# Performance work log

Measured on AMD Instinct MI355X. Metric: run time of the kernel, lower is better.

## Reference

```python
import jax, jax.numpy as jnp
import numpy as np

B, N, C, L = 32, 1024, 1024, 16  # batch, pixels (HW), channels, visual tokens


def setup_inputs() -> dict:
    key = jax.random.key(0)
    ks = jax.random.split(key, 18)
    s = lambda fan_in: 1.0 / np.sqrt(fan_in)
    def lin(kw, kb, fin, fout):
        W = jax.random.uniform(kw, (fin, fout), jnp.float32, -s(fin), s(fin))
        b = jax.random.uniform(kb, (fout,), jnp.float32, -s(fin), s(fin))
        return W, b
    tok_W, tok_b = lin(ks[0], ks[1], C, L)          # tokenizer pointwise conv
    key_W, key_b = lin(ks[2], ks[3], C, C // 2)     # transformer key proj
    query_W, query_b = lin(ks[4], ks[5], C, C // 2) # transformer query proj
    f1_W, f1_b = lin(ks[6], ks[7], C, C)            # FFN 1
    f2_W, f2_b = lin(ks[8], ks[9], C, C)            # FFN 2
    q_W, q_b = lin(ks[10], ks[11], C, C)            # projector W_q
    k_W, k_b = lin(ks[12], ks[13], C, C)            # projector W_k
    feature_map = jax.random.normal(ks[14], (B, N, C), jnp.float32)
    T_in = jnp.zeros((B, L, C), jnp.float32)  # unused by FilterBasedTokenizer
    return dict(feature_map=feature_map, T_in=T_in,
                tok_W=tok_W, tok_b=tok_b, key_W=key_W, key_b=key_b,
                query_W=query_W, query_b=query_b, f1_W=f1_W, f1_b=f1_b,
                f2_W=f2_W, f2_b=f2_b, q_W=q_W, q_b=q_b, k_W=k_W, k_b=k_b)


def reference(feature_map, T_in, tok_W, tok_b, key_W, key_b, query_W, query_b,
              f1_W, f1_b, f2_W, f2_b, q_W, q_b, k_W, k_b):
    X = feature_map  # [B, N, C]
    # --- FilterBasedTokenizer: softmax over pixel dim, aggregate pixels -> tokens
    proj = X @ tok_W + tok_b                         # [B, N, L]
    attn = jax.nn.softmax(proj, axis=1)              # softmax over N (dim=1)
    T = jnp.einsum('bnl,bnc->blc', attn, X)          # [B, L, C]
    # --- Transformer block on visual tokens
    k = T @ key_W + key_b                            # [B, L, C/2]
    q = T @ query_W + query_b                        # [B, L, C/2]
    scores = jnp.einsum('bld,bmd->blm', k, q)        # [B, L, L]
    T_dash = T + jax.nn.softmax(scores, axis=2) @ T  # self-attn residual
    T_out = T_dash + (jax.nn.relu(T_dash @ f1_W + f1_b) @ f2_W + f2_b)
    # --- Projector: pixels attend to tokens
    sim = jnp.einsum('bnc,blc->bnl', X @ q_W + q_b, T_out @ k_W + k_b)  # [B, N, L]
    X_out = X + jax.nn.softmax(sim, axis=2) @ T_out  # [B, N, C]
    return (X_out, T_out)
```

## Files before the change

### kernel.cpp

```cpp
#include <hip/hip_runtime.h>
#include <hip/hip_bf16.h>
#include <stdint.h>

#define BB 32
#define NN 1024
#define CC 1024
#define LL 16

typedef __attribute__((ext_vector_type(4))) float f32x4;
typedef __attribute__((ext_vector_type(8))) short short8;
typedef __attribute__((ext_vector_type(4))) unsigned short ushort4v;

__device__ __forceinline__ unsigned short f2bf(float f) {
  union { float f; unsigned u; } v; v.f = f;
  unsigned r = v.u + 0x7FFF + ((v.u >> 16) & 1);
  return (unsigned short)(r >> 16);
}
__device__ __forceinline__ float bf2f(unsigned short h) {
  union { unsigned u; float f; } v; v.u = ((unsigned)h) << 16; return v.f;
}

__global__ __launch_bounds__(256) void wprep(
    const float* __restrict__ keyW, const float* __restrict__ queryW,
    const float* __restrict__ f1W, const float* __restrict__ f2W,
    const float* __restrict__ kW, const float* __restrict__ qW,
    const float* __restrict__ tokW, const float* __restrict__ keyb,
    const float* __restrict__ queryb,
    unsigned short* __restrict__ WkqT, unsigned short* __restrict__ f1WT,
    unsigned short* __restrict__ f2WT, unsigned short* __restrict__ kWT,
    unsigned short* __restrict__ qWbf, unsigned short* __restrict__ tokWT,
    float* __restrict__ biaskq)
{
  int z = blockIdx.z;
  int tx = threadIdx.x, ty = threadIdx.y;
  if (z == 5) {
    int gid = (blockIdx.y * 32 + blockIdx.x) * 256 + ty * 32 + tx;
    if (gid < 16384) {
      int l = gid >> 10, c = gid & 1023;
      tokWT[gid] = f2bf(tokW[c * 16 + l]);
    } else if (gid < 17408) {
      int i = gid - 16384;
      biaskq[i] = (i < 512) ? keyb[i] : queryb[i - 512];
    }
    return;
  }
  if (z == 4) {
#pragma unroll
    for (int i = 0; i < 4; ++i) {
      int row = blockIdx.y * 32 + ty + 8 * i;
      int col = blockIdx.x * 32 + tx;
      qWbf[row * 1024 + col] = f2bf(qW[row * 1024 + col]);
    }
    return;
  }
  __shared__ float tile[32][33];
  int j0 = blockIdx.x * 32, k0 = blockIdx.y * 32;
  const float* src = (z == 1) ? f1W : (z == 2) ? f2W : kW;
#pragma unroll
  for (int i = 0; i < 4; ++i) {
    int k = k0 + ty + 8 * i;
    int j = j0 + tx;
    float v;
    if (z == 0) v = (j < 512) ? keyW[k * 512 + j] : queryW[k * 512 + (j - 512)];
    else        v = src[k * 1024 + j];
    tile[ty + 8 * i][tx] = v;
  }
  __syncthreads();
  unsigned short* dst = (z == 0) ? WkqT : (z == 1) ? f1WT : (z == 2) ? f2WT : kWT;
#pragma unroll
  for (int i = 0; i < 4; ++i) {
    int j = j0 + ty + 8 * i;
    dst[j * 1024 + k0 + tx] = f2bf(tile[tx][ty + 8 * i]);
  }
}

__global__ __launch_bounds__(256) void proj_mfma(
    const float* __restrict__ X, const unsigned short* __restrict__ Wt,
    const float* __restrict__ bias, float* __restrict__ out)
{
  __shared__ __align__(16) char sp[16384];
  int tid = threadIdx.x, wid = tid >> 6, lane = tid & 63;
  int lr = lane & 15, hi = lane >> 4;
  int pix0 = blockIdx.x * 64;
  int b = pix0 >> 10;
  int row = tid >> 2, seg = tid & 3;
  const float* xr = X + (size_t)(pix0 + row) * 1024 + seg * 32;
  const unsigned short* Wb = Wt + (size_t)lr * 1024 + hi * 8;
  int wbyte[4];
#pragma unroll
  for (int u = 0; u < 4; ++u)
    wbyte[u] = row * 256 + (((seg * 64 + u * 16) ^ ((row & 7) << 4)));
  int arow = wid * 16 + lr;
  int rbyte = arow * 256;
  int rx = (arow & 7) << 4;
  f32x4 acc = (f32x4)0.f;
  for (int k0 = 0; k0 < 1024; k0 += 128) {
    f32x4 v[8];
#pragma unroll
    for (int i = 0; i < 8; ++i) v[i] = *(const f32x4*)(xr + k0 + i * 4);
    __syncthreads();
#pragma unroll
    for (int u = 0; u < 4; ++u) {
      short8 pk;
      pk[0] = (short)f2bf(v[2*u][0]);   pk[1] = (short)f2bf(v[2*u][1]);
      pk[2] = (short)f2bf(v[2*u][2]);   pk[3] = (short)f2bf(v[2*u][3]);
      pk[4] = (short)f2bf(v[2*u+1][0]); pk[5] = (short)f2bf(v[2*u+1][1]);
      pk[6] = (short)f2bf(v[2*u+1][2]); pk[7] = (short)f2bf(v[2*u+1][3]);
      *(short8*)(sp + wbyte[u]) = pk;
    }
    __syncthreads();
#pragma unroll
    for (int kk = 0; kk < 4; ++kk) {
      short8 af = *(const short8*)(sp + rbyte + (((kk * 64 + hi * 16) ^ rx)));
      short8 bf = *(const short8*)(Wb + k0 + kk * 32);
      acc = __builtin_amdgcn_mfma_f32_16x16x32_bf16(af, bf, acc, 0, 0, 0);
    }
  }
  int pixb = pix0 + wid * 16 + hi * 4;
  float bv = bias[lr];
#pragma unroll
  for (int rr = 0; rr < 4; ++rr) {
    int pix = pixb + rr;
    out[((size_t)b * 16 + lr) * 1024 + (pix & 1023)] = acc[rr] + bv;
  }
}

__global__ __launch_bounds__(256) void softmax_n(float* __restrict__ projT) {
  float* row = projT + (size_t)blockIdx.x * NN;
  int t = threadIdx.x;
  f32x4 v = ((f32x4*)row)[t];
  float m = fmaxf(fmaxf(v[0], v[1]), fmaxf(v[2], v[3]));
#pragma unroll
  for (int msk = 32; msk >= 1; msk >>= 1) m = fmaxf(m, __shfl_xor(m, msk));
  __shared__ float redm[4], reds[4];
  if ((t & 63) == 0) redm[t >> 6] = m;
  __syncthreads();
  m = fmaxf(fmaxf(redm[0], redm[1]), fmaxf(redm[2], redm[3]));
  f32x4 e;
  e[0] = __expf(v[0] - m); e[1] = __expf(v[1] - m);
  e[2] = __expf(v[2] - m); e[3] = __expf(v[3] - m);
  float s = e[0] + e[1] + e[2] + e[3];
#pragma unroll
  for (int msk = 32; msk >= 1; msk >>= 1) s += __shfl_xor(s, msk);
  if ((t & 63) == 0) reds[t >> 6] = s;
  __syncthreads();
  s = reds[0] + reds[1] + reds[2] + reds[3];
  float inv = 1.f / s;
  e[0] *= inv; e[1] *= inv; e[2] *= inv; e[3] *= inv;
  ((f32x4*)row)[t] = e;
}

__global__ __launch_bounds__(256) void tpart_kernel(
    const float* __restrict__ X, const float* __restrict__ attnT,
    unsigned short* __restrict__ TpartBf)
{
  int b = blockIdx.y, ch = blockIdx.x;
  int n0 = ch * 128;
  __shared__ float att[128][16];
  int tid = threadIdx.x;
#pragma unroll
  for (int i = 0; i < 2; ++i) {
    int fi = tid + 256 * i;
    int l = fi >> 5, n4 = (fi & 31) << 2;
    f32x4 a = *(const f32x4*)&attnT[((size_t)b * 16 + l) * 1024 + n0 + n4];
    att[n4 + 0][l] = a[0]; att[n4 + 1][l] = a[1];
    att[n4 + 2][l] = a[2]; att[n4 + 3][l] = a[3];
  }
  __syncthreads();
  f32x4 acc[16];
#pragma unroll
  for (int l = 0; l < 16; ++l) acc[l] = (f32x4)0.f;
  const float* xp = X + ((size_t)b * 1024 + n0) * 1024 + tid * 4;
#pragma unroll 4
  for (int n = 0; n < 128; ++n) {
    f32x4 xv = *(const f32x4*)(xp + (size_t)n * 1024);
    const f32x4* ar = (const f32x4*)&att[n][0];
    f32x4 a0 = ar[0], a1 = ar[1], a2 = ar[2], a3 = ar[3];
    acc[0]  += a0[0]*xv; acc[1]  += a0[1]*xv; acc[2]  += a0[2]*xv; acc[3]  += a0[3]*xv;
    acc[4]  += a1[0]*xv; acc[5]  += a1[1]*xv; acc[6]  += a1[2]*xv; acc[7]  += a1[3]*xv;
    acc[8]  += a2[0]*xv; acc[9]  += a2[1]*xv; acc[10] += a2[2]*xv; acc[11] += a2[3]*xv;
    acc[12] += a3[0]*xv; acc[13] += a3[1]*xv; acc[14] += a3[2]*xv; acc[15] += a3[3]*xv;
  }
  unsigned short* op = TpartBf + (size_t)(b * 8 + ch) * 16 * 1024 + tid * 4;
#pragma unroll
  for (int l = 0; l < 16; ++l) {
    f32x4 s = acc[l];
    ushort4v h; h[0]=f2bf(s[0]); h[1]=f2bf(s[1]); h[2]=f2bf(s[2]); h[3]=f2bf(s[3]);
    *(ushort4v*)(op + (size_t)l * 1024) = h;
  }
}

__global__ void treduce(const unsigned short* __restrict__ TpartBf,
                        float* __restrict__ T, unsigned short* __restrict__ Tbf) {
  int f = blockIdx.x * 256 + threadIdx.x;
  int b = f >> 12, w = f & 4095;
  f32x4 s = (f32x4)0.f;
#pragma unroll
  for (int ch = 0; ch < 8; ++ch) {
    ushort4v h = ((const ushort4v*)TpartBf)[(size_t)(b * 8 + ch) * 4096 + w];
    s[0] += bf2f(h[0]); s[1] += bf2f(h[1]); s[2] += bf2f(h[2]); s[3] += bf2f(h[3]);
  }
  ((f32x4*)T)[f] = s;
  ushort4v h; h[0]=f2bf(s[0]); h[1]=f2bf(s[1]); h[2]=f2bf(s[2]); h[3]=f2bf(s[3]);
  ((ushort4v*)Tbf)[f] = h;
}

template<int RELU, int HAS_BIAS, int HAS_RES, int STORE_F32, int STORE_BF16>
__global__ __launch_bounds__(256) void gemm32x64(
    const unsigned short* __restrict__ A, const unsigned short* __restrict__ Bm,
    const float* __restrict__ bias, const float* __restrict__ res,
    float* __restrict__ outF, unsigned short* __restrict__ outB)
{
  const int K = 1024;
  __shared__ __align__(16) char sh[12288];
  char* Asp = sh;
  char* Bsp = sh + 4096;
  int tid = threadIdx.x, wid = tid >> 6, lane = tid & 63;
  int lr = lane & 15, hi = lane >> 4;
  int m0 = blockIdx.x * 32, n0 = blockIdx.y * 64;
  int arow = tid >> 3, acol = (tid & 7) * 8;
  int brow = tid >> 2, bcol = (tid & 3) * 16;
  const unsigned short* Ap = A + (size_t)(m0 + arow) * K + acol;
  const unsigned short* Bp = Bm + (size_t)(n0 + brow) * K + bcol;
  int aw  = arow * 128 + (((acol * 2) ^ ((arow & 7) << 4)));
  int bw0 = brow * 128 + (((bcol * 2) ^ ((brow & 7) << 4)));
  int bw1 = brow * 128 + ((((bcol * 2) + 16) ^ ((brow & 7) << 4)));
  short8 aR[2]; short8 bR[2][2];
  aR[0]    = *(const short8*)(Ap);
  bR[0][0] = *(const short8*)(Bp);
  bR[0][1] = *(const short8*)(Bp + 8);
  aR[1]    = *(const short8*)(Ap + 64);
  bR[1][0] = *(const short8*)(Bp + 64);
  bR[1][1] = *(const short8*)(Bp + 72);
  f32x4 acc[2];
  acc[0] = (f32x4)0.f; acc[1] = (f32x4)0.f;
  int wm = (wid >> 1) * 16, wn = (wid & 1) * 32;
  int arb = (wm + lr) * 128, arx = ((wm + lr) & 7) << 4;
  for (int s = 0; s < 16; ++s) {
    __syncthreads();
    *(short8*)(Asp + aw)  = aR[s & 1];
    *(short8*)(Bsp + bw0) = bR[s & 1][0];
    *(short8*)(Bsp + bw1) = bR[s & 1][1];
    __syncthreads();
    if (s + 2 < 16) {
      int k0 = (s + 2) * 64;
      aR[s & 1]    = *(const short8*)(Ap + k0);
      bR[s & 1][0] = *(const short8*)(Bp + k0);
      bR[s & 1][1] = *(const short8*)(Bp + k0 + 8);
    }
#pragma unroll
    for (int kk = 0; kk < 2; ++kk) {
      short8 af = *(const short8*)(Asp + arb + (((kk * 64 + hi * 16) ^ arx)));
#pragma unroll
      for (int sn = 0; sn < 2; ++sn) {
        int br = wn + sn * 16 + lr;
        short8 bf = *(const short8*)(Bsp + br * 128 + (((kk * 64 + hi * 16) ^ ((br & 7) << 4))));
        acc[sn] = __builtin_amdgcn_mfma_f32_16x16x32_bf16(af, bf, acc[sn], 0, 0, 0);
      }
    }
  }
  int row0 = m0 + wm + hi * 4;
#pragma unroll
  for (int sn = 0; sn < 2; ++sn) {
    int col = n0 + wn + sn * 16 + lr;
    float bv_ = HAS_BIAS ? bias[col] : 0.f;
#pragma unroll
    for (int rr = 0; rr < 4; ++rr) {
      float x = acc[sn][rr] + bv_;
      if (RELU) x = fmaxf(x, 0.f);
      size_t idx = (size_t)(row0 + rr) * 1024 + col;
      if (HAS_RES) x += res[idx];
      if (STORE_F32) outF[idx] = x;
      if (STORE_BF16) outB[idx] = f2bf(x);
    }
  }
}

__global__ __launch_bounds__(256) void scores_tdash(
    const float* __restrict__ kq, const float* __restrict__ T,
    float* __restrict__ Tdash, unsigned short* __restrict__ Tdbf)
{
  int cs = blockIdx.x, b = blockIdx.y;
  int c0 = cs * 128;
  __shared__ float Ts[16][128];
  int tid = threadIdx.x, lane = tid & 63;
#pragma unroll
  for (int i = 0; i < 2; ++i) {
    int fi = tid + 256 * i;
    int rrow = fi >> 5, c4 = (fi & 31) * 4;
    *(f32x4*)&Ts[rrow][c4] = *(const f32x4*)&T[((size_t)b * 16 + rrow) * 1024 + c0 + c4];
  }
  __syncthreads();
  int l = tid >> 4, m = tid & 15;
  const float* krow = kq + ((size_t)b * 16 + l) * 1024;
  const float* qrow = kq + ((size_t)b * 16 + m) * 1024 + 512;
  float s = 0.f;
#pragma unroll 8
  for (int d = 0; d < 512; d += 4) {
    f32x4 kv = *(const f32x4*)(krow + d);
    f32x4 qv = *(const f32x4*)(qrow + d);
    s += kv[0]*qv[0] + kv[1]*qv[1] + kv[2]*qv[2] + kv[3]*qv[3];
  }
  float mx = s;
  mx = fmaxf(mx, __shfl_xor(mx, 1)); mx = fmaxf(mx, __shfl_xor(mx, 2));
  mx = fmaxf(mx, __shfl_xor(mx, 4)); mx = fmaxf(mx, __shfl_xor(mx, 8));
  float e = __expf(s - mx);
  float sum = e;
  sum += __shfl_xor(sum, 1); sum += __shfl_xor(sum, 2);
  sum += __shfl_xor(sum, 4); sum += __shfl_xor(sum, 8);
  float pv = e / sum;
  float pl[16];
#pragma unroll
  for (int i = 0; i < 16; ++i) pl[i] = __shfl(pv, (lane & 48) + i);
  float* od = Tdash + ((size_t)b * 16 + l) * 1024 + c0;
  unsigned short* ob = Tdbf + ((size_t)b * 16 + l) * 1024 + c0;
#pragma unroll
  for (int h = 0; h < 2; ++h) {
    int c = m * 8 + h * 4;
    f32x4 o = *(const f32x4*)&Ts[l][c];
#pragma unroll
    for (int mm = 0; mm < 16; ++mm) {
      f32x4 tv = *(const f32x4*)&Ts[mm][c];
      o += pl[mm] * tv;
    }
    *(f32x4*)(od + c) = o;
    ushort4v hh; hh[0]=f2bf(o[0]); hh[1]=f2bf(o[1]); hh[2]=f2bf(o[2]); hh[3]=f2bf(o[3]);
    *(ushort4v*)(ob + c) = hh;
  }
}

__global__ __launch_bounds__(256) void r_kernel(
    const unsigned short* __restrict__ Tkbf, const float* __restrict__ qb,
    float* __restrict__ r)
{
  int row = blockIdx.x * 4 + (threadIdx.x >> 6);
  int lane = threadIdx.x & 63;
  const unsigned short* p = Tkbf + (size_t)row * CC;
  float s = 0.f;
#pragma unroll
  for (int h = 0; h < 2; ++h) {
    int d0 = lane * 8 + h * 512;
    short8 v = *(const short8*)&p[d0];
#pragma unroll
    for (int jj = 0; jj < 8; ++jj)
      s += bf2f((unsigned short)v[jj]) * qb[d0 + jj];
  }
#pragma unroll
  for (int msk = 32; msk >= 1; msk >>= 1) s += __shfl_xor(s, msk);
  if (lane == 0) r[row] = s;
}

__global__ __launch_bounds__(256) void sim_out_kernel(
    const float* __restrict__ X, const unsigned short* __restrict__ Gt,
    const float* __restrict__ rbias, const float* __restrict__ Tout,
    float* __restrict__ Xout)
{
  __shared__ __align__(16) char sp[16384];
  __shared__ float Ps[64][16];
  int tid = threadIdx.x, wid = tid >> 6, lane = tid & 63;
  int lr = lane & 15, hi = lane >> 4;
  int pix0 = blockIdx.x * 64 + blockIdx.y * 1024;
  int b = blockIdx.y;
  int row = tid >> 2, seg = tid & 3;
  const float* xr = X + (size_t)(pix0 + row) * 1024 + seg * 32;
  const unsigned short* Wb = Gt + (size_t)b * 16 * 1024 + (size_t)lr * 1024 + hi * 8;
  int wbyte[4];
#pragma unroll
  for (int u = 0; u < 4; ++u)
    wbyte[u] = row * 256 + (((seg * 64 + u * 16) ^ ((row & 7) << 4)));
  int arow = wid * 16 + lr;
  int rbyte = arow * 256;
  int rx = (arow & 7) << 4;
  f32x4 acc = (f32x4)0.f;
  for (int k0 = 0; k0 < 1024; k0 += 128) {
    f32x4 v[8];
#pragma unroll
    for (int i = 0; i < 8; ++i) v[i] = *(const f32x4*)(xr + k0 + i * 4);
    __syncthreads();
#pragma unroll
    for (int u = 0; u < 4; ++u) {
      short8 pk;
      pk[0] = (short)f2bf(v[2*u][0]);   pk[1] = (short)f2bf(v[2*u][1]);
      pk[2] = (short)f2bf(v[2*u][2]);   pk[3] = (short)f2bf(v[2*u][3]);
      pk[4] = (short)f2bf(v[2*u+1][0]); pk[5] = (short)f2bf(v[2*u+1][1]);
      pk[6] = (short)f2bf(v[2*u+1][2]); pk[7] = (short)f2bf(v[2*u+1][3]);
      *(short8*)(sp + wbyte[u]) = pk;
    }
    __syncthreads();
#pragma unroll
    for (int kk = 0; kk < 4; ++kk) {
      short8 af = *(const short8*)(sp + rbyte + (((kk * 64 + hi * 16) ^ rx)));
      short8 bf = *(const short8*)(Wb + k0 + kk * 32);
      acc = __builtin_amdgcn_mfma_f32_16x16x32_bf16(af, bf, acc, 0, 0, 0);
    }
  }
  float bv = rbias[b * 16 + lr];
  int prow = wid * 16 + hi * 4;
#pragma unroll
  for (int rr = 0; rr < 4; ++rr) {
    float vv = acc[rr] + bv;
    float mx = vv;
    mx = fmaxf(mx, __shfl_xor(mx, 1)); mx = fmaxf(mx, __shfl_xor(mx, 2));
    mx = fmaxf(mx, __shfl_xor(mx, 4)); mx = fmaxf(mx, __shfl_xor(mx, 8));
    float e = __expf(vv - mx);
    float ss = e;
    ss += __shfl_xor(ss, 1); ss += __shfl_xor(ss, 2);
    ss += __shfl_xor(ss, 4); ss += __shfl_xor(ss, 8);
    Ps[prow + rr][lr] = e / ss;
  }
  __syncthreads();
  int c4 = tid * 4;
  f32x4 tsr[16];
#pragma unroll
  for (int l = 0; l < 16; ++l)
    tsr[l] = *(const f32x4*)&Tout[((size_t)b * 16 + l) * 1024 + c4];
  const float* xp = X + (size_t)pix0 * 1024 + c4;
  float* op = Xout + (size_t)pix0 * 1024 + c4;
#pragma unroll 2
  for (int n = 0; n < 64; ++n) {
    f32x4 xv = *(const f32x4*)(xp + (size_t)n * 1024);
    const f32x4* pr = (const f32x4*)&Ps[n][0];
    f32x4 p0 = pr[0], p1 = pr[1], p2 = pr[2], p3 = pr[3];
    f32x4 o = xv;
    o += p0[0]*tsr[0];  o += p0[1]*tsr[1];  o += p0[2]*tsr[2];  o += p0[3]*tsr[3];
    o += p1[0]*tsr[4];  o += p1[1]*tsr[5];  o += p1[2]*tsr[6];  o += p1[3]*tsr[7];
    o += p2[0]*tsr[8];  o += p2[1]*tsr[9];  o += p2[2]*tsr[10]; o += p2[3]*tsr[11];
    o += p3[0]*tsr[12]; o += p3[1]*tsr[13]; o += p3[2]*tsr[14]; o += p3[3]*tsr[15];
    *(f32x4*)(op + (size_t)n * 1024) = o;
  }
}

extern "C" void kernel_launch(void* const* d_in, const int* in_sizes, int n_in,
                              void* d_out, int out_size, void* d_ws, size_t ws_size,
                              hipStream_t stream)
{
  const float* X      = (const float*)d_in[0];
  const float* tokW   = (const float*)d_in[2];
  const float* tokB   = (const float*)d_in[3];
  const float* keyW   = (const float*)d_in[4];
  const float* keyB   = (const float*)d_in[5];
  const float* queryW = (const float*)d_in[6];
  const float* queryB = (const float*)d_in[7];
  const float* f1W    = (const float*)d_in[8];
  const float* f1B    = (const float*)d_in[9];
  const float* f2W    = (const float*)d_in[10];
  const float* f2B    = (const float*)d_in[11];
  const float* qW     = (const float*)d_in[12];
  const float* qB     = (const float*)d_in[13];
  const float* kW     = (const float*)d_in[14];
  const float* kB     = (const float*)d_in[15];

  float* Xout = (float*)d_out;
  float* Tout = (float*)d_out + (size_t)BB * NN * CC;

  char* ws = (char*)d_ws;
  size_t off = 0;
  auto alloc_f = [&](size_t n) { float* pp = (float*)(ws + off); off += n * 4; return pp; };
  float* attn   = alloc_f(524288);
  float* Tbuf   = alloc_f(524288);
  float* kqbuf  = alloc_f(524288);
  float* Tdash  = alloc_f(524288);
  float* rbuf   = alloc_f(1024);
  float* biaskq = alloc_f(1024);
  auto alloc_h = [&](size_t n) { unsigned short* pp = (unsigned short*)(ws + off); off += n * 2; return pp; };
  unsigned short* TpartBf = alloc_h(4194304);
  unsigned short* Tbf    = alloc_h(524288);
  unsigned short* Tdbf   = alloc_h(524288);
  unsigned short* Hbf    = alloc_h(524288);
  unsigned short* Toutbf = alloc_h(524288);
  unsigned short* Tkbf   = alloc_h(524288);
  unsigned short* Gtbf   = alloc_h(524288);
  unsigned short* WkqT   = alloc_h(1048576);
  unsigned short* f1WT   = alloc_h(1048576);
  unsigned short* f2WT   = alloc_h(1048576);
  unsigned short* kWT    = alloc_h(1048576);
  unsigned short* qWbf   = alloc_h(1048576);
  unsigned short* tokWT  = alloc_h(16384);
  (void)ws_size; (void)in_sizes; (void)n_in; (void)out_size;

  wprep<<<dim3(32, 32, 6), dim3(32, 8), 0, stream>>>(keyW, queryW, f1W, f2W, kW, qW,
                                                     tokW, keyB, queryB,
                                                     WkqT, f1WT, f2WT, kWT, qWbf, tokWT, biaskq);
  proj_mfma<<<dim3(512), 256, 0, stream>>>(X, tokWT, tokB, attn);
  softmax_n<<<512, 256, 0, stream>>>(attn);
  tpart_kernel<<<dim3(8, 32), 256, 0, stream>>>(X, attn, TpartBf);
  treduce<<<512, 256, 0, stream>>>(TpartBf, Tbuf, Tbf);
  gemm32x64<0,1,0,1,0><<<dim3(16, 16), 256, 0, stream>>>(Tbf, WkqT, biaskq, nullptr, kqbuf, nullptr);
  scores_tdash<<<dim3(8, 32), 256, 0, stream>>>(kqbuf, Tbuf, Tdash, Tdbf);
  gemm32x64<1,1,0,0,1><<<dim3(16, 16), 256, 0, stream>>>(Tdbf, f1WT, f1B, nullptr, nullptr, Hbf);
  gemm32x64<0,1,1,1,1><<<dim3(16, 16), 256, 0, stream>>>(Hbf, f2WT, f2B, Tdash, Tout, Toutbf);
  gemm32x64<0,1,0,0,1><<<dim3(16, 16), 256, 0, stream>>>(Toutbf, kWT, kB, nullptr, nullptr, Tkbf);
  r_kernel<<<128, 256, 0, stream>>>(Tkbf, qB, rbuf);
  gemm32x64<0,0,0,0,1><<<dim3(16, 16), 256, 0, stream>>>(Tkbf, qWbf, nullptr, nullptr, nullptr, Gtbf);
  sim_out_kernel<<<dim3(16, 32), 256, 0, stream>>>(X, Gtbf, rbuf, Tout, Xout);
}
```

Before: 210.6 us.

## Fuse tokenizer projection, softmax and token aggregation with online-softmax merge

Replaces the four-kernel tokenizer (projection GEMM, softmax over pixels, partial aggregation, reduce) with one fused kernel. Each 64-pixel chunk computes local logits, a local max and sum, and unnormalized partial tokens, and a merge kernel then rescales and combines the chunks flash-style. This avoids reading X twice and the round trip of the attention matrix, at the cost of a larger partial buffer (16 chunks) and an extra exp rescale. The final output store also becomes nontemporal.

```diff
diff --git a/kernel.cpp b/kernel.cpp
--- a/kernel.cpp
+++ b/kernel.cpp
@@ -18,6 +18,14 @@
 }
 __device__ __forceinline__ float bf2f(unsigned short h) {
   union { unsigned u; float f; } v; v.u = ((unsigned)h) << 16; return v.f;
+}
+__device__ __forceinline__ short8 cvt8(f32x4 a, f32x4 b) {
+  short8 r;
+  r[0] = (short)f2bf(a[0]); r[1] = (short)f2bf(a[1]);
+  r[2] = (short)f2bf(a[2]); r[3] = (short)f2bf(a[3]);
+  r[4] = (short)f2bf(b[0]); r[5] = (short)f2bf(b[1]);
+  r[6] = (short)f2bf(b[2]); r[7] = (short)f2bf(b[3]);
+  return r;
 }
 
 __global__ __launch_bounds__(256) void wprep(
@@ -74,135 +82,120 @@
   }
 }
 
-__global__ __launch_bounds__(256) void proj_mfma(
-    const float* __restrict__ X, const unsigned short* __restrict__ Wt,
-    const float* __restrict__ bias, float* __restrict__ out)
-{
-  __shared__ __align__(16) char sp[16384];
+__global__ __launch_bounds__(256) void tok_fused(
+    const float* __restrict__ X, const unsigned short* __restrict__ tokWT,
+    const float* __restrict__ tokB, unsigned short* __restrict__ Tp,
+    float* __restrict__ Mloc, float* __restrict__ Sloc)
+{
+  __shared__ float E[64][16];
+  __shared__ float redm[4][16];
+  __shared__ float reds[4][16];
   int tid = threadIdx.x, wid = tid >> 6, lane = tid & 63;
   int lr = lane & 15, hi = lane >> 4;
-  int pix0 = blockIdx.x * 64;
-  int b = pix0 >> 10;
-  int row = tid >> 2, seg = tid & 3;
-  const float* xr = X + (size_t)(pix0 + row) * 1024 + seg * 32;
-  const unsigned short* Wb = Wt + (size_t)lr * 1024 + hi * 8;
-  int wbyte[4];
-#pragma unroll
-  for (int u = 0; u < 4; ++u)
-    wbyte[u] = row * 256 + (((seg * 64 + u * 16) ^ ((row & 7) << 4)));
-  int arow = wid * 16 + lr;
-  int rbyte = arow * 256;
-  int rx = (arow & 7) << 4;
+  int b = blockIdx.y, ch = blockIdx.x;
+  int pix0 = b * 1024 + ch * 64;
+  const float* Ar = X + (size_t)(pix0 + wid * 16 + lr) * 1024 + hi * 8;
+  const unsigned short* Br = tokWT + lr * 1024 + hi * 8;
   f32x4 acc = (f32x4)0.f;
-  for (int k0 = 0; k0 < 1024; k0 += 128) {
-    f32x4 v[8];
-#pragma unroll
-    for (int i = 0; i < 8; ++i) v[i] = *(const f32x4*)(xr + k0 + i * 4);
-    __syncthreads();
-#pragma unroll
-    for (int u = 0; u < 4; ++u) {
-      short8 pk;
-      pk[0] = (short)f2bf(v[2*u][0]);   pk[1] = (short)f2bf(v[2*u][1]);
-      pk[2] = (short)f2bf(v[2*u][2]);   pk[3] = (short)f2bf(v[2*u][3]);
-      pk[4] = (short)f2bf(v[2*u+1][0]); pk[5] = (short)f2bf(v[2*u+1][1]);
-      pk[6] = (short)f2bf(v[2*u+1][2]); pk[7] = (short)f2bf(v[2*u+1][3]);
-      *(short8*)(sp + wbyte[u]) = pk;
-    }
-    __syncthreads();
-#pragma unroll
-    for (int kk = 0; kk < 4; ++kk) {
-      short8 af = *(const short8*)(sp + rbyte + (((kk * 64 + hi * 16) ^ rx)));
-      short8 bf = *(const short8*)(Wb + k0 + kk * 32);
-      acc = __builtin_amdgcn_mfma_f32_16x16x32_bf16(af, bf, acc, 0, 0, 0);
-    }
-  }
-  int pixb = pix0 + wid * 16 + hi * 4;
-  float bv = bias[lr];
-#pragma unroll
-  for (int rr = 0; rr < 4; ++rr) {
-    int pix = pixb + rr;
-    out[((size_t)b * 16 + lr) * 1024 + (pix & 1023)] = acc[rr] + bv;
-  }
-}
-
-__global__ __launch_bounds__(256) void softmax_n(float* __restrict__ projT) {
-  float* row = projT + (size_t)blockIdx.x * NN;
-  int t = threadIdx.x;
-  f32x4 v = ((f32x4*)row)[t];
-  float m = fmaxf(fmaxf(v[0], v[1]), fmaxf(v[2], v[3]));
-#pragma unroll
-  for (int msk = 32; msk >= 1; msk >>= 1) m = fmaxf(m, __shfl_xor(m, msk));
-  __shared__ float redm[4], reds[4];
-  if ((t & 63) == 0) redm[t >> 6] = m;
+#pragma unroll 4
+  for (int k0 = 0; k0 < 1024; k0 += 32) {
+    f32x4 x0 = *(const f32x4*)(Ar + k0);
+    f32x4 x1 = *(const f32x4*)(Ar + k0 + 4);
+    short8 bfrag = *(const short8*)(Br + k0);
+    acc = __builtin_amdgcn_mfma_f32_16x16x32_bf16(cvt8(x0, x1), bfrag, acc, 0, 0, 0);
+  }
+  float tb = tokB[lr];
+  float sv[4];
+#pragma unroll
+  for (int rr = 0; rr < 4; ++rr) sv[rr] = acc[rr] + tb;
+  float pm = fmaxf(fmaxf(sv[0], sv[1]), fmaxf(sv[2], sv[3]));
+  pm = fmaxf(pm, __shfl_xor(pm, 16));
+  pm = fmaxf(pm, __shfl_xor(pm, 32));
+  if (hi == 0) redm[wid][lr] = pm;
   __syncthreads();
-  m = fmaxf(fmaxf(redm[0], redm[1]), fmaxf(redm[2], redm[3]));
-  f32x4 e;
-  e[0] = __expf(v[0] - m); e[1] = __expf(v[1] - m);
-  e[2] = __expf(v[2] - m); e[3] = __expf(v[3] - m);
-  float s = e[0] + e[1] + e[2] + e[3];
-#pragma unroll
-  for (int msk = 32; msk >= 1; msk >>= 1) s += __shfl_xor(s, msk);
-  if ((t & 63) == 0) reds[t >> 6] = s;
+  float m = fmaxf(fmaxf(redm[0][lr], redm[1][lr]), fmaxf(redm[2][lr], redm[3][lr]));
+  float ev[4]; float ps = 0.f;
+#pragma unroll
+  for (int i = 0; i < 4; ++i) { ev[i] = __expf(sv[i] - m); ps += ev[i]; }
+  ps += __shfl_xor(ps, 16); ps += __shfl_xor(ps, 32);
+  if (hi == 0) reds[wid][lr] = ps;
+#pragma unroll
+  for (int rr = 0; rr < 4; ++rr)
+    E[wid * 16 + hi * 4 + rr][lr] = ev[rr];
   __syncthreads();
-  s = reds[0] + reds[1] + reds[2] + reds[3];
-  float inv = 1.f / s;
-  e[0] *= inv; e[1] *= inv; e[2] *= inv; e[3] *= inv;
-  ((f32x4*)row)[t] = e;
-}
-
-__global__ __launch_bounds__(256) void tpart_kernel(
-    const float* __restrict__ X, const float* __restrict__ attnT,
-    unsigned short* __restrict__ TpartBf)
-{
-  int b = blockIdx.y, ch = blockIdx.x;
-  int n0 = ch * 128;
-  __shared__ float att[128][16];
-  int tid = threadIdx.x;
-#pragma unroll
-  for (int i = 0; i < 2; ++i) {
-    int fi = tid + 256 * i;
-    int l = fi >> 5, n4 = (fi & 31) << 2;
-    f32x4 a = *(const f32x4*)&attnT[((size_t)b * 16 + l) * 1024 + n0 + n4];
-    att[n4 + 0][l] = a[0]; att[n4 + 1][l] = a[1];
-    att[n4 + 2][l] = a[2]; att[n4 + 3][l] = a[3];
-  }
-  __syncthreads();
-  f32x4 acc[16];
-#pragma unroll
-  for (int l = 0; l < 16; ++l) acc[l] = (f32x4)0.f;
-  const float* xp = X + ((size_t)b * 1024 + n0) * 1024 + tid * 4;
-#pragma unroll 4
-  for (int n = 0; n < 128; ++n) {
-    f32x4 xv = *(const f32x4*)(xp + (size_t)n * 1024);
-    const f32x4* ar = (const f32x4*)&att[n][0];
-    f32x4 a0 = ar[0], a1 = ar[1], a2 = ar[2], a3 = ar[3];
-    acc[0]  += a0[0]*xv; acc[1]  += a0[1]*xv; acc[2]  += a0[2]*xv; acc[3]  += a0[3]*xv;
-    acc[4]  += a1[0]*xv; acc[5]  += a1[1]*xv; acc[6]  += a1[2]*xv; acc[7]  += a1[3]*xv;
-    acc[8]  += a2[0]*xv; acc[9]  += a2[1]*xv; acc[10] += a2[2]*xv; acc[11] += a2[3]*xv;
-    acc[12] += a3[0]*xv; acc[13] += a3[1]*xv; acc[14] += a3[2]*xv; acc[15] += a3[3]*xv;
-  }
-  unsigned short* op = TpartBf + (size_t)(b * 8 + ch) * 16 * 1024 + tid * 4;
+  if (tid < 16) {
+    float sl = reds[0][tid] + reds[1][tid] + reds[2][tid] + reds[3][tid];
+    Mloc[(b * 16 + ch) * 16 + tid] = m;
+    Sloc[(b * 16 + ch) * 16 + tid] = sl;
+  }
+  f32x4 a16[16];
+#pragma unroll
+  for (int l = 0; l < 16; ++l) a16[l] = (f32x4)0.f;
+  const float* xp = X + (size_t)pix0 * 1024 + tid * 4;
+  for (int n0 = 0; n0 < 64; n0 += 8) {
+    f32x4 xv[8];
+#pragma unroll
+    for (int i = 0; i < 8; ++i) xv[i] = *(const f32x4*)(xp + (size_t)(n0 + i) * 1024);
+#pragma unroll
+    for (int i = 0; i < 8; ++i) {
+      const f32x4* ar = (const f32x4*)&E[n0 + i][0];
+      f32x4 a0 = ar[0], a1 = ar[1], a2 = ar[2], a3 = ar[3];
+      f32x4 x0 = xv[i];
+      a16[0]  += a0[0]*x0; a16[1]  += a0[1]*x0; a16[2]  += a0[2]*x0; a16[3]  += a0[3]*x0;
+      a16[4]  += a1[0]*x0; a16[5]  += a1[1]*x0; a16[6]  += a1[2]*x0; a16[7]  += a1[3]*x0;
+      a16[8]  += a2[0]*x0; a16[9]  += a2[1]*x0; a16[10] += a2[2]*x0; a16[11] += a2[3]*x0;
+      a16[12] += a3[0]*x0; a16[13] += a3[1]*x0; a16[14] += a3[2]*x0; a16[15] += a3[3]*x0;
+    }
+  }
+  unsigned short* op = Tp + ((size_t)(b * 16 + ch) * 16) * 1024 + tid * 4;
 #pragma unroll
   for (int l = 0; l < 16; ++l) {
-    f32x4 s = acc[l];
+    f32x4 s = a16[l];
     ushort4v h; h[0]=f2bf(s[0]); h[1]=f2bf(s[1]); h[2]=f2bf(s[2]); h[3]=f2bf(s[3]);
     *(ushort4v*)(op + (size_t)l * 1024) = h;
   }
 }
 
-__global__ void treduce(const unsigned short* __restrict__ TpartBf,
-                        float* __restrict__ T, unsigned short* __restrict__ Tbf) {
-  int f = blockIdx.x * 256 + threadIdx.x;
-  int b = f >> 12, w = f & 4095;
-  f32x4 s = (f32x4)0.f;
-#pragma unroll
-  for (int ch = 0; ch < 8; ++ch) {
-    ushort4v h = ((const ushort4v*)TpartBf)[(size_t)(b * 8 + ch) * 4096 + w];
-    s[0] += bf2f(h[0]); s[1] += bf2f(h[1]); s[2] += bf2f(h[2]); s[3] += bf2f(h[3]);
-  }
-  ((f32x4*)T)[f] = s;
-  ushort4v h; h[0]=f2bf(s[0]); h[1]=f2bf(s[1]); h[2]=f2bf(s[2]); h[3]=f2bf(s[3]);
-  ((ushort4v*)Tbf)[f] = h;
+__global__ __launch_bounds__(256) void tmerge(
+    const unsigned short* __restrict__ Tp, const float* __restrict__ Mloc,
+    const float* __restrict__ Sloc, float* __restrict__ T,
+    unsigned short* __restrict__ Tbf)
+{
+  int tid = threadIdx.x;
+  int g = blockIdx.x * 2 + (tid >> 7);
+  int b = g >> 4, l = g & 15;
+  int j = tid & 127;
+  float M = -1e30f;
+#pragma unroll
+  for (int ch = 0; ch < 16; ++ch) M = fmaxf(M, Mloc[(b * 16 + ch) * 16 + l]);
+  float w[16]; float denom = 0.f;
+#pragma unroll
+  for (int ch = 0; ch < 16; ++ch) {
+    w[ch] = __expf(Mloc[(b * 16 + ch) * 16 + l] - M);
+    denom += w[ch] * Sloc[(b * 16 + ch) * 16 + l];
+  }
+  float inv = 1.f / denom;
+  float o[8];
+#pragma unroll
+  for (int t = 0; t < 8; ++t) o[t] = 0.f;
+#pragma unroll
+  for (int ch = 0; ch < 16; ++ch) {
+    const unsigned short* p = Tp + ((size_t)((b * 16 + ch) * 16 + l)) * 1024 + j * 8;
+    short8 v = *(const short8*)p;
+    float wc = w[ch];
+#pragma unroll
+    for (int t = 0; t < 8; ++t) o[t] += wc * bf2f((unsigned short)v[t]);
+  }
+  f32x4 o0, o1; short8 hb;
+#pragma unroll
+  for (int t = 0; t < 4; ++t) {
+    float x0 = o[t] * inv, x1 = o[4 + t] * inv;
+    o0[t] = x0; o1[t] = x1;
+    hb[t] = (short)f2bf(x0); hb[4 + t] = (short)f2bf(x1);
+  }
+  *(f32x4*)(T + (size_t)g * 1024 + j * 8) = o0;
+  *(f32x4*)(T + (size_t)g * 1024 + j * 8 + 4) = o1;
+  *(short8*)(Tbf + (size_t)g * 1024 + j * 8) = hb;
 }
 
 template<int RELU, int HAS_BIAS, int HAS_RES, int STORE_F32, int STORE_BF16>
@@ -426,7 +419,7 @@
     o += p1[0]*tsr[4];  o += p1[1]*tsr[5];  o += p1[2]*tsr[6];  o += p1[3]*tsr[7];
     o += p2[0]*tsr[8];  o += p2[1]*tsr[9];  o += p2[2]*tsr[10]; o += p2[3]*tsr[11];
     o += p3[0]*tsr[12]; o += p3[1]*tsr[13]; o += p3[2]*tsr[14]; o += p3[3]*tsr[15];
-    *(f32x4*)(op + (size_t)n * 1024) = o;
+    __builtin_nontemporal_store(o, (f32x4*)(op + (size_t)n * 1024));
   }
 }
 
@@ -456,14 +449,15 @@
   char* ws = (char*)d_ws;
   size_t off = 0;
   auto alloc_f = [&](size_t n) { float* pp = (float*)(ws + off); off += n * 4; return pp; };
-  float* attn   = alloc_f(524288);
   float* Tbuf   = alloc_f(524288);
   float* kqbuf  = alloc_f(524288);
   float* Tdash  = alloc_f(524288);
   float* rbuf   = alloc_f(1024);
   float* biaskq = alloc_f(1024);
+  float* Mloc   = alloc_f(8192);
+  float* Sloc   = alloc_f(8192);
   auto alloc_h = [&](size_t n) { unsigned short* pp = (unsigned short*)(ws + off); off += n * 2; return pp; };
-  unsigned short* TpartBf = alloc_h(4194304);
+  unsigned short* Tp     = alloc_h(8388608);
   unsigned short* Tbf    = alloc_h(524288);
   unsigned short* Tdbf   = alloc_h(524288);
   unsigned short* Hbf    = alloc_h(524288);
@@ -481,10 +475,8 @@
   wprep<<<dim3(32, 32, 6), dim3(32, 8), 0, stream>>>(keyW, queryW, f1W, f2W, kW, qW,
                                                      tokW, keyB, queryB,
                                                      WkqT, f1WT, f2WT, kWT, qWbf, tokWT, biaskq);
-  proj_mfma<<<dim3(512), 256, 0, stream>>>(X, tokWT, tokB, attn);
-  softmax_n<<<512, 256, 0, stream>>>(attn);
-  tpart_kernel<<<dim3(8, 32), 256, 0, stream>>>(X, attn, TpartBf);
-  treduce<<<512, 256, 0, stream>>>(TpartBf, Tbuf, Tbf);
+  tok_fused<<<dim3(16, 32), 256, 0, stream>>>(X, tokWT, tokB, Tp, Mloc, Sloc);
+  tmerge<<<256, 256, 0, stream>>>(Tp, Mloc, Sloc, Tbuf, Tbf);
   gemm32x64<0,1,0,1,0><<<dim3(16, 16), 256, 0, stream>>>(Tbf, WkqT, biaskq, nullptr, kqbuf, nullptr);
   scores_tdash<<<dim3(8, 32), 256, 0, stream>>>(kqbuf, Tbuf, Tdash, Tdbf);
   gemm32x64<1,1,0,0,1><<<dim3(16, 16), 256, 0, stream>>>(Tdbf, f1WT, f1B, nullptr, nullptr, Hbf);
```

Result: faster. 178.2 us (-15.4%).
